# Kernel optimization log

Measured on AMD Instinct MI355X. Metric: run time of the kernel, lower is better.

## Reference

```python
import jax, jax.numpy as jnp
import numpy as np

NUM_HOPS = 4
N_NODES = 50000
N_EDGES = 500000
D = 128
H1 = 256
INIT_A, INIT_B = -0.01, 0.01


def _mlp(x, w1, b1, w2, b2):
    # Linear -> ReLU -> Linear -> ReLU (Dropout is identity in eval mode)
    h = jax.nn.relu(x @ w1 + b1)
    return jax.nn.relu(h @ w2 + b2)


def _uniform(key, shape):
    return jax.random.uniform(key, shape, jnp.float32, INIT_A, INIT_B)


def setup_inputs() -> dict:
    key = jax.random.key(0)
    ks = jax.random.split(key, 40)
    inp = {
        "batch_token": jax.random.normal(ks[0], (N_NODES, D), jnp.float32),
        "edge_p_node": jax.random.randint(ks[1], (N_EDGES,), 0, N_NODES),
        "edge_c_node": jax.random.randint(ks[2], (N_EDGES,), 0, N_NODES),
        "edge_p_indicate": jax.random.uniform(ks[3], (N_EDGES,), jnp.float32),
        "edge_c_indicate": jax.random.uniform(ks[4], (N_EDGES,), jnp.float32),
        "p_mask": jax.random.uniform(ks[5], (N_NODES,), jnp.float32),
        "c_mask": jax.random.uniform(ks[6], (N_NODES,), jnp.float32),
        "start_token": jax.random.normal(ks[7], (D,), jnp.float32),
        "end_token": jax.random.normal(ks[8], (D,), jnp.float32),
    }
    # MLP_V: D -> H1 -> D ; MLP_E: 1 -> H1 -> D ; MLP_p/c/aggr: 3D -> H1 -> D
    k = 9
    for name, din in (("V", D), ("E", 1), ("P", 3 * D), ("C", 3 * D), ("A", 3 * D)):
        inp[name + "w1"] = _uniform(ks[k], (din, H1)); k += 1
        inp[name + "b1"] = _uniform(ks[k], (H1,)); k += 1
        inp[name + "w2"] = _uniform(ks[k], (H1, D)); k += 1
        inp[name + "b2"] = _uniform(ks[k], (D,)); k += 1
    return inp


def reference(batch_token, edge_p_node, edge_c_node, edge_p_indicate,
              edge_c_indicate, p_mask, c_mask, start_token, end_token,
              Vw1, Vb1, Vw2, Vb2, Ew1, Eb1, Ew2, Eb2,
              Pw1, Pb1, Pw2, Pb2, Cw1, Cb1, Cw2, Cb2,
              Aw1, Ab1, Aw2, Ab2):
    n = batch_token.shape[0]
    h = _mlp(batch_token, Vw1, Vb1, Vw2, Vb2)  # [N, D]
    edge_p = _mlp(edge_p_indicate[:, None], Ew1, Eb1, Ew2, Eb2)  # [E, D]
    edge_c = _mlp(edge_c_indicate[:, None], Ew1, Eb1, Ew2, Eb2)  # [E, D]
    ones_e = jnp.ones((edge_p_node.shape[0],), jnp.float32)
    cnt_p = jnp.clip(jax.ops.segment_sum(ones_e, edge_p_node, num_segments=n), 1.0)
    cnt_c = jnp.clip(jax.ops.segment_sum(ones_e, edge_c_node, num_segments=n), 1.0)
    for _ in range(NUM_HOPS - 1):
        hp = h[edge_p_node]  # [E, D]
        hc = h[edge_c_node]  # [E, D]
        s_p = _mlp(jnp.concatenate([hc, hp, edge_p], -1), Pw1, Pb1, Pw2, Pb2)
        s_c = _mlp(jnp.concatenate([hp, hc, edge_c], -1), Cw1, Cb1, Cw2, Cb2)
        s_p = jax.ops.segment_sum(s_p, edge_p_node, num_segments=n) / cnt_p[:, None]
        s_c = jax.ops.segment_sum(s_c, edge_c_node, num_segments=n) / cnt_c[:, None]
        s_p = s_p + p_mask[:, None] * start_token
        s_c = s_c + c_mask[:, None] * end_token
        x_aggr = jnp.concatenate([h, s_p, s_c], -1)  # [N, 3D]
        h = jax.nn.relu(h + _mlp(x_aggr, Aw1, Ab1, Aw2, Ab2))
    return h
```

## Files before the change

### kernel.cpp

```cpp
#include <hip/hip_runtime.h>
#include <hip/hip_bf16.h>
#include <cstdint>
#include <cstddef>
#include <cmath>

typedef __bf16 bf16;
typedef bf16 bf16x8 __attribute__((ext_vector_type(8)));
typedef float f32x4 __attribute__((ext_vector_type(4)));

#define D_DIM 128
#define NB 32
#define EB 64
#define TS 136
#define XS 264
#define SRS 132
#define AS 392

__device__ __forceinline__ f32x4 mfma16(bf16x8 a, bf16x8 b, f32x4 c) {
  return __builtin_amdgcn_mfma_f32_16x16x32_bf16(a, b, c, 0, 0, 0);
}

__device__ __forceinline__ int clampi(int v, int hi) {
  return v < 0 ? 0 : (v > hi ? hi : v);
}

__device__ __forceinline__ void stage16(const float* __restrict__ src, bf16* dst) {
  bf16 tmp[16];
#pragma unroll
  for (int q = 0; q < 4; ++q) {
    f32x4 f = ((const f32x4*)src)[q];
#pragma unroll
    for (int j = 0; j < 4; ++j) tmp[q * 4 + j] = (bf16)f[j];
  }
  *(bf16x8*)dst = *(bf16x8*)tmp;
  *(bf16x8*)(dst + 8) = *(bf16x8*)(tmp + 8);
}

template <int NSEG>
__device__ __forceinline__ void mlp_layer1(const bf16* s0, const bf16* s1, const bf16* s2,
                                           const int S,
                                           const bf16* __restrict__ W1t,
                                           const float* __restrict__ B1,
                                           bf16* x2, const int lane, const int w) {
  const int col = lane & 15, quad = lane >> 4;
  const int K = NSEG * 128;
  f32x4 acc[2][4] = {};
  const bf16* segs[3] = {s0, s1, s2};
#pragma unroll
  for (int sg = 0; sg < NSEG; ++sg) {
    const bf16* xl = segs[sg];
#pragma unroll
    for (int kk = 0; kk < 128; kk += 32) {
      const int k0 = sg * 128 + kk;
      bf16x8 a0 = *(const bf16x8*)&xl[col * S + kk + quad * 8];
      bf16x8 a1 = *(const bf16x8*)&xl[(col + 16) * S + kk + quad * 8];
#pragma unroll
      for (int nt = 0; nt < 4; ++nt) {
        bf16x8 b = *(const bf16x8*)(W1t + (size_t)(w * 64 + nt * 16 + col) * K + k0 + quad * 8);
        acc[0][nt] = mfma16(a0, b, acc[0][nt]);
        acc[1][nt] = mfma16(a1, b, acc[1][nt]);
      }
    }
  }
#pragma unroll
  for (int nt = 0; nt < 4; ++nt) {
    const int n = w * 64 + nt * 16 + col;
    const float b1 = B1[n];
#pragma unroll
    for (int mt = 0; mt < 2; ++mt)
#pragma unroll
      for (int i = 0; i < 4; ++i) {
        float v = acc[mt][nt][i] + b1;
        x2[(mt * 16 + quad * 4 + i) * XS + n] = (bf16)(v > 0.f ? v : 0.f);
      }
  }
}

__device__ __forceinline__ void mlp_layer2(const bf16* x2, const bf16* __restrict__ W2t,
                                           const int lane, const int w, f32x4 acc2[2][2]) {
  const int col = lane & 15, quad = lane >> 4;
#pragma unroll
  for (int k0 = 0; k0 < 256; k0 += 32) {
    bf16x8 a0 = *(const bf16x8*)&x2[col * XS + k0 + quad * 8];
    bf16x8 a1 = *(const bf16x8*)&x2[(col + 16) * XS + k0 + quad * 8];
#pragma unroll
    for (int nt = 0; nt < 2; ++nt) {
      bf16x8 b = *(const bf16x8*)(W2t + (size_t)(w * 32 + nt * 16 + col) * 256 + k0 + quad * 8);
      acc2[0][nt] = mfma16(a0, b, acc2[0][nt]);
      acc2[1][nt] = mfma16(a1, b, acc2[1][nt]);
    }
  }
}

__device__ __forceinline__ void emit_z(const bf16* x, const int S,
                                       const bf16* __restrict__ Pw1t,
                                       const bf16* __restrict__ Cw1t,
                                       bf16* __restrict__ Zbuf,
                                       const int r0, const int N,
                                       const int lane, const int w) {
  const int col = lane & 15, quad = lane >> 4;
  const bf16* base = ((w & 2) ? Cw1t : Pw1t) + (w & 1) * 128;
  bf16* out = Zbuf + (size_t)w * ((size_t)N * 256);
#pragma unroll
  for (int half = 0; half < 2; ++half) {
    f32x4 acc[2][8] = {};
#pragma unroll
    for (int kc = 0; kc < 4; ++kc) {
      bf16x8 a0 = *(const bf16x8*)&x[col * S + kc * 32 + quad * 8];
      bf16x8 a1 = *(const bf16x8*)&x[(col + 16) * S + kc * 32 + quad * 8];
#pragma unroll
      for (int nt = 0; nt < 8; ++nt) {
        const int n = half * 128 + nt * 16 + col;
        bf16x8 b = *(const bf16x8*)(base + (size_t)n * 384 + kc * 32 + quad * 8);
        acc[0][nt] = mfma16(a0, b, acc[0][nt]);
        acc[1][nt] = mfma16(a1, b, acc[1][nt]);
      }
    }
#pragma unroll
    for (int nt = 0; nt < 8; ++nt) {
      const int n = half * 128 + nt * 16 + col;
#pragma unroll
      for (int mt = 0; mt < 2; ++mt)
#pragma unroll
        for (int i = 0; i < 4; ++i) {
          int g = r0 + mt * 16 + quad * 4 + i;
          if (g < N) out[(size_t)g * 256 + n] = (bf16)acc[mt][nt][i];
        }
    }
  }
}


__global__ void transpose_kernel(const float* __restrict__ in, bf16* __restrict__ out,
                                 int K, int N) {
  int k = blockIdx.x * blockDim.x + threadIdx.x;
  int n = blockIdx.y;
  if (k < K) out[(size_t)n * K + k] = (bf16)in[(size_t)k * N + n];
}

__global__ void count_kernel(const int* __restrict__ epn, const int* __restrict__ ecn,
                             int* cntp, int* cntc, int E, int N) {
  int i = blockIdx.x * blockDim.x + threadIdx.x;
  if (i < E) {
    atomicAdd(&cntp[clampi(epn[i], N - 1)], 1);
    atomicAdd(&cntc[clampi(ecn[i], N - 1)], 1);
  }
}

__global__ void inv_kernel(const int* __restrict__ cntp, const int* __restrict__ cntc,
                           float* invp, float* invc, int N) {
  int i = blockIdx.x * blockDim.x + threadIdx.x;
  if (i < N) {
    invp[i] = 1.f / fmaxf((float)cntp[i], 1.f);
    invc[i] = 1.f / fmaxf((float)cntc[i], 1.f);
  }
}

__global__ void scan_pair_kernel(const int* __restrict__ cntp, const int* __restrict__ cntc,
                                 int* __restrict__ offp, int* __restrict__ offc, int n) {
  const int* cnt = blockIdx.x ? cntc : cntp;
  int* offs = blockIdx.x ? offc : offp;
  __shared__ int buf[1024];
  __shared__ int carry;
  const int t = threadIdx.x;
  if (t == 0) carry = 0;
  __syncthreads();
  for (int base = 0; base < n; base += 1024) {
    int v = (base + t < n) ? cnt[base + t] : 0;
    buf[t] = v;
    __syncthreads();
    for (int d = 1; d < 1024; d <<= 1) {
      int add = (t >= d) ? buf[t - d] : 0;
      __syncthreads();
      buf[t] += add;
      __syncthreads();
    }
    if (base + t < n) offs[base + t] = carry + buf[t] - v;
    __syncthreads();
    if (t == 1023) carry += buf[1023];
    __syncthreads();
  }
}

__global__ void scatter_kernel(const int* __restrict__ epn, const int* __restrict__ ecn,
                               const int* __restrict__ offp, const int* __restrict__ offc,
                               int* curp, int* curc, int* sortp, int* sortc, int E, int N) {
  int i = blockIdx.x * blockDim.x + threadIdx.x;
  if (i < E) {
    int p = clampi(epn[i], N - 1);
    sortp[offp[p] + atomicAdd(&curp[p], 1)] = i;
    int c = clampi(ecn[i], N - 1);
    sortc[offc[c] + atomicAdd(&curc[c], 1)] = i;
  }
}


__global__ __launch_bounds__(256) void emlp_table_kernel(
    const float* __restrict__ Ew1, const float* __restrict__ Eb1,
    const float* __restrict__ Ew2, const float* __restrict__ Eb2,
    float* __restrict__ ts_out, float* __restrict__ Atab, float* __restrict__ Btab) {
  __shared__ float s_tk[256], s_w[256], s_b[256];
  __shared__ int s_k[256];
  __shared__ float sA[256], sB[256];
  const int j = blockIdx.x;
  const int t = threadIdx.x;
  float w = Ew1[t], b = Eb1[t];
  float tk = (w != 0.f) ? (-b / w) : INFINITY;
  s_tk[t] = tk; s_w[t] = w; s_b[t] = b;
  __syncthreads();
  int rank = 0;
  for (int u = 0; u < 256; ++u) {
    float tu = s_tk[u];
    if (tu < tk || (tu == tk && u < t)) ++rank;
  }
  s_k[rank] = t;
  if (j == 0) ts_out[rank] = tk;
  float w2own = Ew2[(size_t)t * 128 + j];
  bool act = (w < 0.f || (w == 0.f && b > 0.f));
  sA[t] = act ? w * w2own : 0.f;
  sB[t] = act ? b * w2own : 0.f;
  __syncthreads();
  for (int d = 128; d > 0; d >>= 1) {
    if (t < d) { sA[t] += sA[t + d]; sB[t] += sB[t + d]; }
    __syncthreads();
  }
  const float baseA = sA[0], baseB = sB[0];
  __syncthreads();
  int k = s_k[t];
  float wk = s_w[k], bk = s_b[k];
  float dA = 0.f, dB = 0.f;
  if (wk != 0.f) {
    float w2 = Ew2[(size_t)k * 128 + j];
    float sgn = wk > 0.f ? 1.f : -1.f;
    dA = sgn * wk * w2;
    dB = sgn * bk * w2;
  }
  sA[t] = dA; sB[t] = dB;
  __syncthreads();
  for (int d = 1; d < 256; d <<= 1) {
    float aA = (t >= d) ? sA[t - d] : 0.f;
    float aB = (t >= d) ? sB[t - d] : 0.f;
    __syncthreads();
    sA[t] += aA; sB[t] += aB;
    __syncthreads();
  }
  const float eb2 = Eb2[j];
  if (t == 0) { Atab[j] = baseA; Btab[j] = baseB + eb2; }
  Atab[(size_t)(t + 1) * 128 + j] = baseA + sA[t];
  Btab[(size_t)(t + 1) * 128 + j] = baseB + sB[t] + eb2;
}


__global__ __launch_bounds__(256, 3) void node_v_kernel(
    const float* __restrict__ bt, const bf16* __restrict__ W1t, const float* __restrict__ B1,
    const bf16* __restrict__ W2t, const float* __restrict__ B2,
    const bf16* __restrict__ Pw1t, const bf16* __restrict__ Cw1t,
    bf16* __restrict__ Zbuf, float* __restrict__ hout, int N) {
  __shared__ __attribute__((aligned(16))) bf16 x[NB * TS];
  __shared__ __attribute__((aligned(16))) bf16 x2[NB * XS];
  const int t = threadIdx.x;
  const int r0 = blockIdx.x * NB;
  {
    const int r = t >> 3, c0 = (t & 7) * 16;
    int g = r0 + r; if (g >= N) g = N - 1;
    stage16(bt + (size_t)g * D_DIM + c0, &x[r * TS + c0]);
  }
  __syncthreads();
  const int lane = t & 63, w = t >> 6, col = lane & 15, quad = lane >> 4;
  mlp_layer1<1>(x, x, x, TS, W1t, B1, x2, lane, w);
  __syncthreads();
  f32x4 acc2[2][2] = {};
  mlp_layer2(x2, W2t, lane, w, acc2);
  __syncthreads();
#pragma unroll
  for (int nt = 0; nt < 2; ++nt) {
    const int n = w * 32 + nt * 16 + col;
    const float b2 = B2[n];
#pragma unroll
    for (int mt = 0; mt < 2; ++mt)
#pragma unroll
      for (int i = 0; i < 4; ++i) {
        int m = mt * 16 + quad * 4 + i;
        int g = r0 + m;
        float v = acc2[mt][nt][i] + b2;
        v = v > 0.f ? v : 0.f;
        x[m * TS + n] = (bf16)v;
        if (g < N) hout[(size_t)g * D_DIM + n] = v;
      }
  }
  __syncthreads();
  emit_z(x, TS, Pw1t, Cw1t, Zbuf, r0, N, lane, w);
}


__global__ __launch_bounds__(512, 6) void edge_side_kernel(
    const bf16* __restrict__ Zbuf,
    const float* __restrict__ epi, const float* __restrict__ eci,
    const int* __restrict__ epn, const int* __restrict__ ecn,
    const int* __restrict__ sortp, const int* __restrict__ sortc,
    const float* __restrict__ ets, const float* __restrict__ Atab,
    const float* __restrict__ Btab,
    const bf16* __restrict__ Pw1t, const float* __restrict__ Pb1,
    const bf16* __restrict__ Pw2t, const float* __restrict__ Pb2,
    const bf16* __restrict__ Cw1t, const float* __restrict__ Cb1,
    const bf16* __restrict__ Cw2t, const float* __restrict__ Cb2,
    float* __restrict__ accp, float* __restrict__ accc, int E, int N) {
  const int side = blockIdx.y;
  const size_t NZ = (size_t)N * 256;
  const bf16* ZO     = Zbuf + (size_t)(side * 2 + 0) * NZ;
  const bf16* ZW     = Zbuf + (size_t)(side * 2 + 1) * NZ;
  const float* ei    = side ? eci : epi;
  const int* own_n   = side ? ecn : epn;
  const int* oth_n   = side ? epn : ecn;
  const int* sorted  = side ? sortc : sortp;
  const bf16* W1c    = (side ? Cw1t : Pw1t) + 256;
  const float* B1    = side ? Cb1 : Pb1;
  const bf16* W2t    = side ? Cw2t : Pw2t;
  const float* B2    = side ? Cb2 : Pb2;
  float* acc         = side ? accc : accp;

  __shared__ int s_own[EB], s_oth[EB];
  __shared__ float s_x[EB];
  __shared__ float s_ts[256];
  __shared__ __attribute__((aligned(16))) bf16 feat[EB * TS];
  __shared__ __attribute__((aligned(16))) char xbuf[EB * XS * 2];
  bf16* xz = (bf16*)xbuf;
  float* sred = (float*)xbuf;

  const int t = threadIdx.x;
  const int e0 = blockIdx.x * EB;
  if (t < 256) s_ts[t] = ets[t];
  if (t < EB) {
    int e = e0 + t;
    if (e < E) {
      int id = clampi(sorted[e], E - 1);
      s_own[t] = clampi(own_n[id], N - 1);
      s_oth[t] = clampi(oth_n[id], N - 1);
      s_x[t] = ei[id];
    } else {
      s_own[t] = -1; s_oth[t] = 0; s_x[t] = 0.f;
    }
  }
  __syncthreads();

  const int lane = t & 63, w = t >> 6, col = lane & 15, quad = lane >> 4;

  bf16x8 va[4];
  const int zr = t >> 3, zc = (t & 7) * 32;
  const bf16* pw_s;
  {
    int ro = s_oth[zr];
    const bf16* po = ZO + (size_t)ro * 256 + zc;
#pragma unroll
    for (int q = 0; q < 4; ++q) va[q] = *(const bf16x8*)(po + q * 8);
    int rw = s_own[zr]; if (rw < 0) rw = 0;
    pw_s = ZW + (size_t)rw * 256 + zc;
  }

  {
    const int r = zr, c0 = (t & 7) * 16;
    const float xv = s_x[r];
    int lo = 0, hi = 256;
#pragma unroll
    for (int it = 0; it < 8; ++it) {
      int mid = (lo + hi) >> 1;
      if (s_ts[mid] < xv) lo = mid + 1; else hi = mid;
    }
    const float* Ar = Atab + (size_t)lo * 128 + c0;
    const float* Br = Btab + (size_t)lo * 128 + c0;
#pragma unroll
    for (int q = 0; q < 2; ++q) {
      f32x4 a0 = *(const f32x4*)(Ar + q * 8);
      f32x4 a1 = *(const f32x4*)(Ar + q * 8 + 4);
      f32x4 b0 = *(const f32x4*)(Br + q * 8);
      f32x4 b1v = *(const f32x4*)(Br + q * 8 + 4);
      bf16 o[8];
#pragma unroll
      for (int j = 0; j < 4; ++j) {
        float v0 = fmaf(xv, a0[j], b0[j]);
        float v1 = fmaf(xv, a1[j], b1v[j]);
        o[j] = (bf16)(v0 > 0.f ? v0 : 0.f);
        o[4 + j] = (bf16)(v1 > 0.f ? v1 : 0.f);
      }
      *(bf16x8*)&feat[r * TS + c0 + q * 8] = *(bf16x8*)o;
    }
  }

  {
#pragma unroll
    for (int q = 0; q < 4; ++q) {
      bf16x8 b = *(const bf16x8*)(pw_s + q * 8);
      bf16 o[8];
#pragma unroll
      for (int j = 0; j < 8; ++j) o[j] = (bf16)((float)va[q][j] + (float)b[j]);
      *(bf16x8*)&xz[zr * XS + zc + q * 8] = *(bf16x8*)o;
    }
  }
  __syncthreads();

  {
    f32x4 acc1[4][2] = {};
#pragma unroll
    for (int kc = 0; kc < 4; ++kc) {
      bf16x8 afr[4];
#pragma unroll
      for (int g = 0; g < 4; ++g)
        afr[g] = *(const bf16x8*)&feat[(g * 16 + col) * TS + kc * 32 + quad * 8];
#pragma unroll
      for (int nt = 0; nt < 2; ++nt) {
        const int n = w * 32 + nt * 16 + col;
        bf16x8 b = *(const bf16x8*)(W1c + (size_t)n * 384 + kc * 32 + quad * 8);
#pragma unroll
        for (int g = 0; g < 4; ++g) acc1[g][nt] = mfma16(afr[g], b, acc1[g][nt]);
      }
    }
#pragma unroll
    for (int nt = 0; nt < 2; ++nt) {
      const int n = w * 32 + nt * 16 + col;
      const float b1 = B1[n];
#pragma unroll
      for (int g = 0; g < 4; ++g)
#pragma unroll
        for (int i = 0; i < 4; ++i) {
          const int m = g * 16 + quad * 4 + i;
          float v = acc1[g][nt][i] + b1 + (float)xz[m * XS + n];
          xz[m * XS + n] = (bf16)(v > 0.f ? v : 0.f);
        }
    }
  }
  __syncthreads();

  f32x4 acc2[4];
#pragma unroll
  for (int g = 0; g < 4; ++g) acc2[g] = (f32x4){0.f, 0.f, 0.f, 0.f};
#pragma unroll
  for (int kc = 0; kc < 8; ++kc) {
    bf16x8 afr[4];
#pragma unroll
    for (int g = 0; g < 4; ++g)
      afr[g] = *(const bf16x8*)&xz[(g * 16 + col) * XS + kc * 32 + quad * 8];
    const int n = w * 16 + col;
    bf16x8 b = *(const bf16x8*)(W2t + (size_t)n * 256 + kc * 32 + quad * 8);
#pragma unroll
    for (int g = 0; g < 4; ++g) acc2[g] = mfma16(afr[g], b, acc2[g]);
  }
  __syncthreads();

  {
    const int n = w * 16 + col;
    const float b2 = B2[n];
#pragma unroll
    for (int g = 0; g < 4; ++g)
#pragma unroll
      for (int i = 0; i < 4; ++i) {
        float v = acc2[g][i] + b2;
        sred[(g * 16 + quad * 4 + i) * SRS + n] = v > 0.f ? v : 0.f;
      }
  }
  __syncthreads();
  {
    const int c = w * 16 + (lane >> 2);
    const int rlo = (lane & 3) * 16;
    float run = 0.f;
    int cur = s_own[rlo];
    for (int r = rlo; r < rlo + 16; ++r) {
      int k = s_own[r];
      if (k != cur) {
        if (cur >= 0)
          __hip_atomic_fetch_add(&acc[(size_t)cur * D_DIM + c], run,
                                 __ATOMIC_RELAXED, __HIP_MEMORY_SCOPE_AGENT);
        run = 0.f;
        cur = k;
      }
      run += sred[r * SRS + c];
    }
    if (cur >= 0)
      __hip_atomic_fetch_add(&acc[(size_t)cur * D_DIM + c], run,
                             __ATOMIC_RELAXED, __HIP_MEMORY_SCOPE_AGENT);
  }
}


__global__ __launch_bounds__(256, 3) void node_a_kernel(
    const float* __restrict__ h, const float* __restrict__ accp, const float* __restrict__ accc,
    const float* __restrict__ invp, const float* __restrict__ invc,
    const float* __restrict__ pmask, const float* __restrict__ cmask,
    const float* __restrict__ stok, const float* __restrict__ etok,
    const bf16* __restrict__ W1t, const float* __restrict__ B1,
    const bf16* __restrict__ W2t, const float* __restrict__ B2,
    const bf16* __restrict__ Pw1t, const bf16* __restrict__ Cw1t,
    bf16* __restrict__ Zbuf, int emitZ,
    float* __restrict__ hout, int N) {
  __shared__ __attribute__((aligned(16))) bf16 x[NB * AS];
  __shared__ __attribute__((aligned(16))) bf16 x2[NB * XS];
  const int t = threadIdx.x;
  const int r0 = blockIdx.x * NB;
  {
    const int r = t >> 3, c0 = (t & 7) * 16;
    int g = r0 + r; if (g >= N) g = N - 1;
    stage16(h + (size_t)g * D_DIM + c0, &x[r * AS + c0]);
  }
  {
    const int j = t;
    for (int r = 0; r < NB; ++r) {
      int g = r0 + r; if (g >= N) g = N - 1;
      float v;
      if (j < 128)
        v = accp[(size_t)g * D_DIM + j] * invp[g] + pmask[g] * stok[j];
      else {
        int jj = j - 128;
        v = accc[(size_t)g * D_DIM + jj] * invc[g] + cmask[g] * etok[jj];
      }
      x[r * AS + 128 + j] = (bf16)v;
    }
  }
  __syncthreads();
  const int lane = t & 63, w = t >> 6, col = lane & 15, quad = lane >> 4;
  mlp_layer1<3>(x, x + 128, x + 256, AS, W1t, B1, x2, lane, w);
  __syncthreads();
  f32x4 acc2[2][2] = {};
  mlp_layer2(x2, W2t, lane, w, acc2);
  __syncthreads();
#pragma unroll
  for (int nt = 0; nt < 2; ++nt) {
    const int n = w * 32 + nt * 16 + col;
    const float b2 = B2[n];
#pragma unroll
    for (int mt = 0; mt < 2; ++mt)
#pragma unroll
      for (int i = 0; i < 4; ++i) {
        int m = mt * 16 + quad * 4 + i;
        int g = r0 + m;
        int gc = g < N ? g : N - 1;
        float mlpv = acc2[mt][nt][i] + b2;
        mlpv = mlpv > 0.f ? mlpv : 0.f;
        float v = h[(size_t)gc * D_DIM + n] + mlpv;
        v = v > 0.f ? v : 0.f;
        x[m * AS + n] = (bf16)v;
        if (g < N) hout[(size_t)g * D_DIM + n] = v;
      }
  }
  if (emitZ) {
    __syncthreads();
    emit_z(x, AS, Pw1t, Cw1t, Zbuf, r0, N, lane, w);
  }
}


extern "C" void kernel_launch(void* const* d_in, const int* in_sizes, int n_in,
                              void* d_out, int out_size, void* d_ws, size_t ws_size,
                              hipStream_t stream) {
  const float* batch_token = (const float*)d_in[0];
  const int* epn = (const int*)d_in[1];
  const int* ecn = (const int*)d_in[2];
  const float* epi = (const float*)d_in[3];
  const float* eci = (const float*)d_in[4];
  const float* pmask = (const float*)d_in[5];
  const float* cmask = (const float*)d_in[6];
  const float* stok = (const float*)d_in[7];
  const float* etok = (const float*)d_in[8];
  const float *Vw1 = (const float*)d_in[9], *Vb1 = (const float*)d_in[10],
              *Vw2 = (const float*)d_in[11], *Vb2 = (const float*)d_in[12];
  const float *Ew1 = (const float*)d_in[13], *Eb1 = (const float*)d_in[14],
              *Ew2 = (const float*)d_in[15], *Eb2 = (const float*)d_in[16];
  const float *Pw1 = (const float*)d_in[17], *Pb1 = (const float*)d_in[18],
              *Pw2 = (const float*)d_in[19], *Pb2 = (const float*)d_in[20];
  const float *Cw1 = (const float*)d_in[21], *Cb1 = (const float*)d_in[22],
              *Cw2 = (const float*)d_in[23], *Cb2 = (const float*)d_in[24];
  const float *Aw1 = (const float*)d_in[25], *Ab1 = (const float*)d_in[26],
              *Aw2 = (const float*)d_in[27], *Ab2 = (const float*)d_in[28];
  const int N = in_sizes[5];
  const int E = in_sizes[1];

  char* ws = (char*)d_ws;
  size_t off = 0;
  auto alloc = [&](size_t bytes) {
    size_t o = off;
    off += (bytes + 511) & ~(size_t)511;
    return o;
  };
  float* accp = (float*)(ws + alloc((size_t)N * D_DIM * 4));
  float* accc = (float*)(ws + alloc((size_t)N * D_DIM * 4));
  bf16* Zbuf = (bf16*)(ws + alloc((size_t)4 * N * 256 * 2));
  float* invp = (float*)(ws + alloc((size_t)N * 4));
  float* invc = (float*)(ws + alloc((size_t)N * 4));
  int* cntp = (int*)(ws + alloc((size_t)N * 4));
  int* cntc = (int*)(ws + alloc((size_t)N * 4));
  int* offp = (int*)(ws + alloc((size_t)N * 4));
  int* offc = (int*)(ws + alloc((size_t)N * 4));
  int* curp = (int*)(ws + alloc((size_t)N * 4));
  int* curc = (int*)(ws + alloc((size_t)N * 4));
  int* sortp = (int*)(ws + alloc((size_t)E * 4));
  int* sortc = (int*)(ws + alloc((size_t)E * 4));
  bf16* Vw1t = (bf16*)(ws + alloc(128 * 256 * 2));
  bf16* Pw1t = (bf16*)(ws + alloc(384 * 256 * 2));
  bf16* Cw1t = (bf16*)(ws + alloc(384 * 256 * 2));
  bf16* Aw1t = (bf16*)(ws + alloc(384 * 256 * 2));
  bf16* Vw2t = (bf16*)(ws + alloc(256 * 128 * 2));
  bf16* Pw2t = (bf16*)(ws + alloc(256 * 128 * 2));
  bf16* Cw2t = (bf16*)(ws + alloc(256 * 128 * 2));
  bf16* Aw2t = (bf16*)(ws + alloc(256 * 128 * 2));
  float* ets  = (float*)(ws + alloc(256 * 4));
  float* Atab = (float*)(ws + alloc((size_t)257 * 128 * 4));
  float* Btab = (float*)(ws + alloc((size_t)257 * 128 * 4));
  float* hbuf = (float*)d_out;
  (void)ws_size; (void)n_in; (void)out_size;

  const dim3 blk(256);
  transpose_kernel<<<dim3(1, 256), blk, 0, stream>>>(Vw1, Vw1t, 128, 256);
  transpose_kernel<<<dim3(2, 256), blk, 0, stream>>>(Pw1, Pw1t, 384, 256);
  transpose_kernel<<<dim3(2, 256), blk, 0, stream>>>(Cw1, Cw1t, 384, 256);
  transpose_kernel<<<dim3(2, 256), blk, 0, stream>>>(Aw1, Aw1t, 384, 256);
  transpose_kernel<<<dim3(1, 128), blk, 0, stream>>>(Vw2, Vw2t, 256, 128);
  transpose_kernel<<<dim3(1, 128), blk, 0, stream>>>(Pw2, Pw2t, 256, 128);
  transpose_kernel<<<dim3(1, 128), blk, 0, stream>>>(Cw2, Cw2t, 256, 128);
  transpose_kernel<<<dim3(1, 128), blk, 0, stream>>>(Aw2, Aw2t, 256, 128);

  emlp_table_kernel<<<dim3(128), dim3(256), 0, stream>>>(Ew1, Eb1, Ew2, Eb2, ets, Atab, Btab);

  const size_t cntbytes = (size_t)((char*)(cntc + N) - (char*)cntp);
  hipMemsetAsync(cntp, 0, cntbytes, stream);
  count_kernel<<<dim3((E + 255) / 256), blk, 0, stream>>>(epn, ecn, cntp, cntc, E, N);
  inv_kernel<<<dim3((N + 255) / 256), blk, 0, stream>>>(cntp, cntc, invp, invc, N);
  scan_pair_kernel<<<dim3(2), dim3(1024), 0, stream>>>(cntp, cntc, offp, offc, N);
  const size_t curbytes = (size_t)((char*)(curc + N) - (char*)curp);
  hipMemsetAsync(curp, 0, curbytes, stream);
  scatter_kernel<<<dim3((E + 255) / 256), blk, 0, stream>>>(epn, ecn, offp, offc,
                                                            curp, curc, sortp, sortc, E, N);

  const int nblocks = (N + NB - 1) / NB;
  const int eblocks = (E + EB - 1) / EB;

  node_v_kernel<<<dim3(nblocks), blk, 0, stream>>>(
      batch_token, Vw1t, Vb1, Vw2t, Vb2, Pw1t, Cw1t, Zbuf, hbuf, N);

  const size_t accbytes = (size_t)((char*)(accc + (size_t)N * D_DIM) - (char*)accp);
  for (int hop = 0; hop < 3; ++hop) {
    hipMemsetAsync(accp, 0, accbytes, stream);
    edge_side_kernel<<<dim3(eblocks, 2), dim3(512), 0, stream>>>(
        Zbuf, epi, eci, epn, ecn, sortp, sortc, ets, Atab, Btab,
        Pw1t, Pb1, Pw2t, Pb2, Cw1t, Cb1, Cw2t, Cb2, accp, accc, E, N);
    node_a_kernel<<<dim3(nblocks), blk, 0, stream>>>(
        hbuf, accp, accc, invp, invc, pmask, cmask, stok, etok,
        Aw1t, Ab1, Aw2t, Ab2, Pw1t, Cw1t, Zbuf, (hop < 2) ? 1 : 0, hbuf, N);
  }
}
```

Baseline: 2.066 ms.

## Split edge MLP hidden dim into two halves to shrink LDS and raise occupancy

The edge-side kernel now processes the 256-wide hidden layer in two 128-column halves. The precomputed Z rows are combined and consumed half at a time, so the second-layer accumulation carries across both halves. This shrinks the shared-memory footprint to one union buffer of two 64x136 bf16 tiles and lowers per-thread accumulator registers. The launch bound is raised from 6 to 8 blocks per CU to allow more resident blocks. In exchange there are extra barriers and the second half of each Z row is loaded separately, which adds some latency.

Result: no change. 2.052 ms (-0.7%).

```diff
diff --git a/kernel.cpp b/kernel.cpp
--- a/kernel.cpp
+++ b/kernel.cpp
@@ -293,7 +293,7 @@
 }
 
 
-__global__ __launch_bounds__(512, 6) void edge_side_kernel(
+__global__ __launch_bounds__(512, 8) void edge_side_kernel(
     const bf16* __restrict__ Zbuf,
     const float* __restrict__ epi, const float* __restrict__ eci,
     const int* __restrict__ epn, const int* __restrict__ ecn,
@@ -322,10 +322,10 @@
   __shared__ int s_own[EB], s_oth[EB];
   __shared__ float s_x[EB];
   __shared__ float s_ts[256];
-  __shared__ __attribute__((aligned(16))) bf16 feat[EB * TS];
-  __shared__ __attribute__((aligned(16))) char xbuf[EB * XS * 2];
-  bf16* xz = (bf16*)xbuf;
-  float* sred = (float*)xbuf;
+  __shared__ __attribute__((aligned(16))) char ubuf[EB * TS * 2 * 2];
+  bf16* feat = (bf16*)ubuf;
+  bf16* xzh  = (bf16*)(ubuf + EB * TS * 2);
+  float* sred = (float*)ubuf;
 
   const int t = threadIdx.x;
   const int e0 = blockIdx.x * EB;
@@ -344,30 +344,30 @@
   __syncthreads();
 
   const int lane = t & 63, w = t >> 6, col = lane & 15, quad = lane >> 4;
-
-  bf16x8 va[4];
-  const int zr = t >> 3, zc = (t & 7) * 32;
-  const bf16* pw_s;
+  const int zr = t >> 3, zc = (t & 7) * 16;
+
+  const bf16* zo_row;
+  const bf16* zw_row;
+  bf16x8 va0, va1;
   {
     int ro = s_oth[zr];
-    const bf16* po = ZO + (size_t)ro * 256 + zc;
-#pragma unroll
-    for (int q = 0; q < 4; ++q) va[q] = *(const bf16x8*)(po + q * 8);
     int rw = s_own[zr]; if (rw < 0) rw = 0;
-    pw_s = ZW + (size_t)rw * 256 + zc;
-  }
-
-  {
-    const int r = zr, c0 = (t & 7) * 16;
-    const float xv = s_x[r];
+    zo_row = ZO + (size_t)ro * 256;
+    zw_row = ZW + (size_t)rw * 256;
+    va0 = *(const bf16x8*)(zo_row + zc);
+    va1 = *(const bf16x8*)(zo_row + zc + 8);
+  }
+
+  {
+    const float xv = s_x[zr];
     int lo = 0, hi = 256;
 #pragma unroll
     for (int it = 0; it < 8; ++it) {
       int mid = (lo + hi) >> 1;
       if (s_ts[mid] < xv) lo = mid + 1; else hi = mid;
     }
-    const float* Ar = Atab + (size_t)lo * 128 + c0;
-    const float* Br = Btab + (size_t)lo * 128 + c0;
+    const float* Ar = Atab + (size_t)lo * 128 + zc;
+    const float* Br = Btab + (size_t)lo * 128 + zc;
 #pragma unroll
     for (int q = 0; q < 2; ++q) {
       f32x4 a0 = *(const f32x4*)(Ar + q * 8);
@@ -382,79 +382,125 @@
         o[j] = (bf16)(v0 > 0.f ? v0 : 0.f);
         o[4 + j] = (bf16)(v1 > 0.f ? v1 : 0.f);
       }
-      *(bf16x8*)&feat[r * TS + c0 + q * 8] = *(bf16x8*)o;
-    }
-  }
-
-  {
-#pragma unroll
-    for (int q = 0; q < 4; ++q) {
-      bf16x8 b = *(const bf16x8*)(pw_s + q * 8);
-      bf16 o[8];
-#pragma unroll
-      for (int j = 0; j < 8; ++j) o[j] = (bf16)((float)va[q][j] + (float)b[j]);
-      *(bf16x8*)&xz[zr * XS + zc + q * 8] = *(bf16x8*)o;
-    }
-  }
-  __syncthreads();
-
-  {
-    f32x4 acc1[4][2] = {};
+      *(bf16x8*)&feat[zr * TS + zc + q * 8] = *(bf16x8*)o;
+    }
+  }
+
+  {
+    bf16x8 b0 = *(const bf16x8*)(zw_row + zc);
+    bf16x8 b1 = *(const bf16x8*)(zw_row + zc + 8);
+    bf16 o0[8], o1[8];
+#pragma unroll
+    for (int j = 0; j < 8; ++j) {
+      o0[j] = (bf16)((float)va0[j] + (float)b0[j]);
+      o1[j] = (bf16)((float)va1[j] + (float)b1[j]);
+    }
+    *(bf16x8*)&xzh[zr * TS + zc] = *(bf16x8*)o0;
+    *(bf16x8*)&xzh[zr * TS + zc + 8] = *(bf16x8*)o1;
+  }
+  __syncthreads();
+
+  va0 = *(const bf16x8*)(zo_row + 128 + zc);
+  va1 = *(const bf16x8*)(zo_row + 128 + zc + 8);
+
+  f32x4 acc2[4];
+#pragma unroll
+  for (int g = 0; g < 4; ++g) acc2[g] = (f32x4){0.f, 0.f, 0.f, 0.f};
+
+  const int nh = w * 16 + col;
+
+  {
+    f32x4 acc1[4] = {};
 #pragma unroll
     for (int kc = 0; kc < 4; ++kc) {
       bf16x8 afr[4];
 #pragma unroll
       for (int g = 0; g < 4; ++g)
         afr[g] = *(const bf16x8*)&feat[(g * 16 + col) * TS + kc * 32 + quad * 8];
-#pragma unroll
-      for (int nt = 0; nt < 2; ++nt) {
-        const int n = w * 32 + nt * 16 + col;
-        bf16x8 b = *(const bf16x8*)(W1c + (size_t)n * 384 + kc * 32 + quad * 8);
-#pragma unroll
-        for (int g = 0; g < 4; ++g) acc1[g][nt] = mfma16(afr[g], b, acc1[g][nt]);
-      }
-    }
-#pragma unroll
-    for (int nt = 0; nt < 2; ++nt) {
-      const int n = w * 32 + nt * 16 + col;
-      const float b1 = B1[n];
+      bf16x8 b = *(const bf16x8*)(W1c + (size_t)nh * 384 + kc * 32 + quad * 8);
+#pragma unroll
+      for (int g = 0; g < 4; ++g) acc1[g] = mfma16(afr[g], b, acc1[g]);
+    }
+    const float b1v = B1[nh];
+#pragma unroll
+    for (int g = 0; g < 4; ++g)
+#pragma unroll
+      for (int i = 0; i < 4; ++i) {
+        const int m = g * 16 + quad * 4 + i;
+        float v = acc1[g][i] + b1v + (float)xzh[m * TS + nh];
+        xzh[m * TS + nh] = (bf16)(v > 0.f ? v : 0.f);
+      }
+  }
+  __syncthreads();
+#pragma unroll
+  for (int kc = 0; kc < 4; ++kc) {
+    bf16x8 afr[4];
+#pragma unroll
+    for (int g = 0; g < 4; ++g)
+      afr[g] = *(const bf16x8*)&xzh[(g * 16 + col) * TS + kc * 32 + quad * 8];
+    bf16x8 b = *(const bf16x8*)(W2t + (size_t)nh * 256 + kc * 32 + quad * 8);
+#pragma unroll
+    for (int g = 0; g < 4; ++g) acc2[g] = mfma16(afr[g], b, acc2[g]);
+  }
+  __syncthreads();
+
+  {
+    bf16x8 b0 = *(const bf16x8*)(zw_row + 128 + zc);
+    bf16x8 b1 = *(const bf16x8*)(zw_row + 128 + zc + 8);
+    bf16 o0[8], o1[8];
+#pragma unroll
+    for (int j = 0; j < 8; ++j) {
+      o0[j] = (bf16)((float)va0[j] + (float)b0[j]);
+      o1[j] = (bf16)((float)va1[j] + (float)b1[j]);
+    }
+    *(bf16x8*)&xzh[zr * TS + zc] = *(bf16x8*)o0;
+    *(bf16x8*)&xzh[zr * TS + zc + 8] = *(bf16x8*)o1;
+  }
+  __syncthreads();
+
+  {
+    f32x4 acc1[4] = {};
+#pragma unroll
+    for (int kc = 0; kc < 4; ++kc) {
+      bf16x8 afr[4];
 #pragma unroll
       for (int g = 0; g < 4; ++g)
-#pragma unroll
-        for (int i = 0; i < 4; ++i) {
-          const int m = g * 16 + quad * 4 + i;
-          float v = acc1[g][nt][i] + b1 + (float)xz[m * XS + n];
-          xz[m * XS + n] = (bf16)(v > 0.f ? v : 0.f);
-        }
-    }
-  }
-  __syncthreads();
-
-  f32x4 acc2[4];
-#pragma unroll
-  for (int g = 0; g < 4; ++g) acc2[g] = (f32x4){0.f, 0.f, 0.f, 0.f};
-#pragma unroll
-  for (int kc = 0; kc < 8; ++kc) {
+        afr[g] = *(const bf16x8*)&feat[(g * 16 + col) * TS + kc * 32 + quad * 8];
+      bf16x8 b = *(const bf16x8*)(W1c + (size_t)(128 + nh) * 384 + kc * 32 + quad * 8);
+#pragma unroll
+      for (int g = 0; g < 4; ++g) acc1[g] = mfma16(afr[g], b, acc1[g]);
+    }
+    const float b1v = B1[128 + nh];
+#pragma unroll
+    for (int g = 0; g < 4; ++g)
+#pragma unroll
+      for (int i = 0; i < 4; ++i) {
+        const int m = g * 16 + quad * 4 + i;
+        float v = acc1[g][i] + b1v + (float)xzh[m * TS + nh];
+        xzh[m * TS + nh] = (bf16)(v > 0.f ? v : 0.f);
+      }
+  }
+  __syncthreads();
+#pragma unroll
+  for (int kc = 0; kc < 4; ++kc) {
     bf16x8 afr[4];
 #pragma unroll
     for (int g = 0; g < 4; ++g)
-      afr[g] = *(const bf16x8*)&xz[(g * 16 + col) * XS + kc * 32 + quad * 8];
-    const int n = w * 16 + col;
-    bf16x8 b = *(const bf16x8*)(W2t + (size_t)n * 256 + kc * 32 + quad * 8);
+      afr[g] = *(const bf16x8*)&xzh[(g * 16 + col) * TS + kc * 32 + quad * 8];
+    bf16x8 b = *(const bf16x8*)(W2t + (size_t)nh * 256 + 128 + kc * 32 + quad * 8);
 #pragma unroll
     for (int g = 0; g < 4; ++g) acc2[g] = mfma16(afr[g], b, acc2[g]);
   }
   __syncthreads();
 
   {
-    const int n = w * 16 + col;
-    const float b2 = B2[n];
+    const float b2 = B2[nh];
 #pragma unroll
     for (int g = 0; g < 4; ++g)
 #pragma unroll
       for (int i = 0; i < 4; ++i) {
         float v = acc2[g][i] + b2;
-        sred[(g * 16 + quad * 4 + i) * SRS + n] = v > 0.f ? v : 0.f;
+        sred[(g * 16 + quad * 4 + i) * SRS + nh] = v > 0.f ? v : 0.f;
       }
   }
   __syncthreads();
```
